# Kernel optimization log

Measured on AMD Instinct MI355X. Metric: run time of the kernel, lower is better.

## Reference

```python
import jax, jax.numpy as jnp
import numpy as np


def setup_inputs() -> dict:
    key = jax.random.key(0)
    k1, k2, k3 = jax.random.split(key, 3)
    N, E, D = 100000, 3200000, 32  # neurons, total edges (fan-in sum), feature dim
    src = jax.random.normal(k1, (N, D), dtype=jnp.float32)
    gather_idx = jax.random.randint(k2, (E,), 0, N, dtype=jnp.int32)
    # repeat_interleave(arange(N), repeats) is nondecreasing -> sorted segment ids
    segment_ids = jnp.sort(jax.random.randint(k3, (E,), 0, N, dtype=jnp.int32))
    return {"src": src, "gather_idx": gather_idx, "segment_ids": segment_ids, "num_segments": N}


def reference(src, gather_idx, segment_ids, num_segments):
    # gather neuron input values: [E, D]
    gathered = src[gather_idx]
    # scatter_mean over variable-length groups (segment mean)
    sums = jax.ops.segment_sum(gathered, segment_ids, num_segments=num_segments,
                               indices_are_sorted=True)
    counts = jax.ops.segment_sum(jnp.ones((gathered.shape[0],), dtype=src.dtype),
                                 segment_ids, num_segments=num_segments,
                                 indices_are_sorted=True)
    return sums / jnp.maximum(counts, 1.0)[:, None]
```

## Files before the change

kernel.cpp:

```cpp
#include <hip/hip_runtime.h>


constexpr int D = 32;
constexpr int GSZ = 8;
constexpr int BLOCK = 256;
constexpr int SEGS_PER_BLOCK = BLOCK / GSZ;

__global__ __launch_bounds__(BLOCK) void seg_bounds_kernel(
    const int* __restrict__ segid,
    int*       __restrict__ start,
    int E, int N)
{
    int e = blockIdx.x * BLOCK + threadIdx.x;
    if (e > E) return;
    int s, p;
    if (e == E) { s = N; p = segid[E - 1]; }
    else        { s = segid[e]; p = (e == 0) ? -1 : segid[e - 1]; }
    for (int n = p + 1; n <= s; ++n) start[n] = e;
}

__global__ __launch_bounds__(BLOCK) void AggregationLayer_53051436040325_kernel(
    const float* __restrict__ src,
    const int*   __restrict__ gidx,
    const int*   __restrict__ start,
    float*       __restrict__ out,
    int N)
{
    const int n   = blockIdx.x * SEGS_PER_BLOCK + (threadIdx.x >> 3);
    const int sub = threadIdx.x & (GSZ - 1);
    if (n >= N) return;

    const int lo = start[n];
    const int hi = start[n + 1];

    const float* srcp = src + (size_t)sub * 4;

    float4 acc = make_float4(0.f, 0.f, 0.f, 0.f);
    int e = lo;
    for (; e + 8 <= hi; e += 8) {
        int g[8];
#pragma unroll
        for (int j = 0; j < 8; ++j) g[j] = gidx[e + j];
        float4 v[8];
#pragma unroll
        for (int j = 0; j < 8; ++j) v[j] = *(const float4*)(srcp + (size_t)g[j] * D);
#pragma unroll
        for (int j = 0; j < 8; ++j) {
            acc.x += v[j].x; acc.y += v[j].y; acc.z += v[j].z; acc.w += v[j].w;
        }
    }
    for (; e < hi; ++e) {
        const int g = gidx[e];
        const float4 v = *(const float4*)(srcp + (size_t)g * D);
        acc.x += v.x; acc.y += v.y; acc.z += v.z; acc.w += v.w;
    }

    const int c = hi - lo;
    const float cnt = (float)(c > 0 ? c : 1);
    float4 r;
    r.x = acc.x / cnt;
    r.y = acc.y / cnt;
    r.z = acc.z / cnt;
    r.w = acc.w / cnt;
    *(float4*)(out + (size_t)n * D + sub * 4) = r;
}

extern "C" void kernel_launch(void* const* d_in, const int* in_sizes, int n_in,
                              void* d_out, int out_size, void* d_ws, size_t ws_size,
                              hipStream_t stream) {
    const float* src   = (const float*)d_in[0];
    const int*   gidx  = (const int*)d_in[1];
    const int*   segid = (const int*)d_in[2];
    const int E = in_sizes[1];
    const int N = in_sizes[0] / D;

    int*   start = (int*)d_ws;
    float* out   = (float*)d_out;

    const int blocksA = (E + 1 + BLOCK - 1) / BLOCK;
    seg_bounds_kernel<<<blocksA, BLOCK, 0, stream>>>(segid, start, E, N);

    const int blocksB = (N + SEGS_PER_BLOCK - 1) / SEGS_PER_BLOCK;
    AggregationLayer_53051436040325_kernel<<<blocksB, BLOCK, 0, stream>>>(src, gidx, start, out, N);
}
```

Measured before the change: 136.3 us.

## Convert source table to fp16 in prep kernel to halve gather bytes

The segment-bounds kernel now also converts the float32 source table to fp16 in workspace, and the aggregation kernel gathers 16-byte half8 rows with four threads per segment instead of eight. Accumulation stays in float32. The goal is to halve the bytes moved by the random row gathers, which dominate traffic. In exchange the extra conversion pass reads and writes the whole table, and fp16 rounding of the inputs adds error to the output.

```diff
diff --git a/kernel.cpp b/kernel.cpp
--- a/kernel.cpp
+++ b/kernel.cpp
@@ -1,68 +1,90 @@
 #include <hip/hip_runtime.h>
+#include <hip/hip_fp16.h>
 
 
 constexpr int D = 32;
-constexpr int GSZ = 8;
+constexpr int GSZ = 4;
 constexpr int BLOCK = 256;
 constexpr int SEGS_PER_BLOCK = BLOCK / GSZ;
 
-__global__ __launch_bounds__(BLOCK) void seg_bounds_kernel(
-    const int* __restrict__ segid,
-    int*       __restrict__ start,
-    int E, int N)
+typedef _Float16 half8 __attribute__((ext_vector_type(8)));
+
+__global__ __launch_bounds__(BLOCK) void prep_kernel(
+    const float* __restrict__ src,
+    const int*   __restrict__ segid,
+    int*         __restrict__ start,
+    _Float16*    __restrict__ hsrc,
+    int E, int N, int total)
 {
-    int e = blockIdx.x * BLOCK + threadIdx.x;
-    if (e > E) return;
-    int s, p;
-    if (e == E) { s = N; p = segid[E - 1]; }
-    else        { s = segid[e]; p = (e == 0) ? -1 : segid[e - 1]; }
-    for (int n = p + 1; n <= s; ++n) start[n] = e;
+    const int e = blockIdx.x * BLOCK + threadIdx.x;
+
+    if (e <= E) {
+        int s, p;
+        if (e == E) { s = N; p = segid[E - 1]; }
+        else        { s = segid[e]; p = (e == 0) ? -1 : segid[e - 1]; }
+        for (int n = p + 1; n <= s; ++n) start[n] = e;
+    }
+
+    const int i = e * 8;
+    if (i < total) {
+        const float4 a = *(const float4*)(src + i);
+        const float4 b = *(const float4*)(src + i + 4);
+        half8 h;
+        h[0] = (_Float16)a.x; h[1] = (_Float16)a.y;
+        h[2] = (_Float16)a.z; h[3] = (_Float16)a.w;
+        h[4] = (_Float16)b.x; h[5] = (_Float16)b.y;
+        h[6] = (_Float16)b.z; h[7] = (_Float16)b.w;
+        *(half8*)(hsrc + i) = h;
+    }
 }
 
 __global__ __launch_bounds__(BLOCK) void AggregationLayer_53051436040325_kernel(
-    const float* __restrict__ src,
-    const int*   __restrict__ gidx,
-    const int*   __restrict__ start,
-    float*       __restrict__ out,
+    const _Float16* __restrict__ hsrc,
+    const int*      __restrict__ gidx,
+    const int*      __restrict__ start,
+    float*          __restrict__ out,
     int N)
 {
-    const int n   = blockIdx.x * SEGS_PER_BLOCK + (threadIdx.x >> 3);
+    const int n   = blockIdx.x * SEGS_PER_BLOCK + (threadIdx.x >> 2);
     const int sub = threadIdx.x & (GSZ - 1);
     if (n >= N) return;
 
     const int lo = start[n];
     const int hi = start[n + 1];
 
-    const float* srcp = src + (size_t)sub * 4;
+    const _Float16* sp = hsrc + sub * 8;
 
-    float4 acc = make_float4(0.f, 0.f, 0.f, 0.f);
+    float acc[8];
+#pragma unroll
+    for (int j = 0; j < 8; ++j) acc[j] = 0.f;
+
     int e = lo;
     for (; e + 8 <= hi; e += 8) {
         int g[8];
 #pragma unroll
-        for (int j = 0; j < 8; ++j) g[j] = gidx[e + j];
-        float4 v[8];
+        for (int k = 0; k < 8; ++k) g[k] = gidx[e + k];
+        half8 v[8];
 #pragma unroll
-        for (int j = 0; j < 8; ++j) v[j] = *(const float4*)(srcp + (size_t)g[j] * D);
+        for (int k = 0; k < 8; ++k) v[k] = *(const half8*)(sp + (size_t)g[k] * D);
 #pragma unroll
-        for (int j = 0; j < 8; ++j) {
-            acc.x += v[j].x; acc.y += v[j].y; acc.z += v[j].z; acc.w += v[j].w;
-        }
+        for (int k = 0; k < 8; ++k)
+#pragma unroll
+            for (int j = 0; j < 8; ++j) acc[j] += (float)v[k][j];
     }
     for (; e < hi; ++e) {
-        const int g = gidx[e];
-        const float4 v = *(const float4*)(srcp + (size_t)g * D);
-        acc.x += v.x; acc.y += v.y; acc.z += v.z; acc.w += v.w;
+        const half8 v = *(const half8*)(sp + (size_t)gidx[e] * D);
+#pragma unroll
+        for (int j = 0; j < 8; ++j) acc[j] += (float)v[j];
     }
 
     const int c = hi - lo;
-    const float cnt = (float)(c > 0 ? c : 1);
-    float4 r;
-    r.x = acc.x / cnt;
-    r.y = acc.y / cnt;
-    r.z = acc.z / cnt;
-    r.w = acc.w / cnt;
-    *(float4*)(out + (size_t)n * D + sub * 4) = r;
+    const float inv = 1.f / (float)(c > 0 ? c : 1);
+    float4 r0, r1;
+    r0.x = acc[0] * inv; r0.y = acc[1] * inv; r0.z = acc[2] * inv; r0.w = acc[3] * inv;
+    r1.x = acc[4] * inv; r1.y = acc[5] * inv; r1.z = acc[6] * inv; r1.w = acc[7] * inv;
+    float* op = out + (size_t)n * D + sub * 8;
+    *(float4*)(op)     = r0;
+    *(float4*)(op + 4) = r1;
 }
 
 extern "C" void kernel_launch(void* const* d_in, const int* in_sizes, int n_in,
@@ -73,13 +95,16 @@
     const int*   segid = (const int*)d_in[2];
     const int E = in_sizes[1];
     const int N = in_sizes[0] / D;
+    const int total = N * D;
 
-    int*   start = (int*)d_ws;
-    float* out   = (float*)d_out;
+    int*      start = (int*)d_ws;
+    _Float16* hsrc  = (_Float16*)((char*)d_ws + ((size_t)(N + 1) * sizeof(int) + 255 & ~(size_t)255));
+
+    float* out = (float*)d_out;
 
     const int blocksA = (E + 1 + BLOCK - 1) / BLOCK;
-    seg_bounds_kernel<<<blocksA, BLOCK, 0, stream>>>(segid, start, E, N);
+    prep_kernel<<<blocksA, BLOCK, 0, stream>>>(src, segid, start, hsrc, E, N, total);
 
     const int blocksB = (N + SEGS_PER_BLOCK - 1) / SEGS_PER_BLOCK;
-    AggregationLayer_53051436040325_kernel<<<blocksB, BLOCK, 0, stream>>>(src, gidx, start, out, N);
+    AggregationLayer_53051436040325_kernel<<<blocksB, BLOCK, 0, stream>>>(hsrc, gidx, start, out, N);
 }
```

Result: faster. 124.7 us (-8.6%).
